# Performance work log

Measured on AMD Instinct MI355X. Metric: run time of the kernel, lower is better.

The kernel has to match this reference:

```python
import jax, jax.numpy as jnp
import numpy as np

B, N, L = 32, 1024, 128
K, D_E, H = 3, 16, 4


def setup_inputs() -> dict:
    key = jax.random.key(0)
    ks = jax.random.split(key, 7)
    return {
        "x": jax.random.normal(ks[0], (B, N, L), jnp.float32),
        # mild scaling on embeddings/projections keeps softmax logits in a sane range
        "psi_emb": jax.random.normal(ks[1], (N, D_E), jnp.float32) * 0.3,
        "psi": jnp.float32(1.0),
        "W_q": jax.random.normal(ks[2], (D_E, H, D_E), jnp.float32) * 0.2,
        "W_k": jax.random.normal(ks[3], (D_E, H, D_E), jnp.float32) * 0.2,
        "attn_alpha": jnp.float32(0.5),
        "F_w": jax.random.normal(ks[4], (H, D_E, K + 1, L), jnp.float32) * 0.1,
        "f_b": jax.random.normal(ks[5], (H, D_E), jnp.float32),
        "head_mix": jnp.ones((H,), jnp.float32),
    }


def reference(x, psi_emb, psi, W_q, W_k, attn_alpha, F_w, f_b, head_mix):
    # x: (B, N, L)
    n = x.shape[1]
    # --- gaussian adjacency: softmax over columns of exp(-psi * ||psi_i - psi_j||^2)
    diff = psi_emb[:, None, :] - psi_emb[None, :, :]          # (N, N, d_e)
    dist2 = jnp.sum(diff * diff, axis=-1)                     # (N, N)
    A_base = jax.nn.softmax(jnp.exp(-psi * dist2), axis=1)    # (N, N)
    # --- per-head attention adjacency
    Q = jnp.einsum('nd,dhm->nhm', psi_emb, W_q)               # (N, H, d_e)
    Kt = jnp.einsum('nd,dhm->nhm', psi_emb, W_k)              # (N, H, d_e)
    scale = 1.0 / jnp.sqrt(jnp.asarray(Q.shape[-1], x.dtype))
    A_attn = jax.nn.softmax(
        jnp.einsum('nhd,mhd->hnm', Q, Kt) * scale, axis=-1)   # (H, N, N)
    # --- sigmoid blend (all heads at once)
    alpha = jax.nn.sigmoid(attn_alpha)
    A_eff = alpha * A_base[None] + (1.0 - alpha) * A_attn     # (H, N, N)
    # --- Chebyshev recursion: T0 = I, T1 = A, Tk = 2 A T_{k-1} - T_{k-2}
    I = jnp.broadcast_to(jnp.eye(n, dtype=x.dtype), A_eff.shape)
    supports = [I, A_eff]
    for _ in range(2, K + 1):
        supports.append(2.0 * jnp.einsum('hnm,hml->hnl', A_eff, supports[-1]) - supports[-2])
    S = jnp.stack(supports, axis=1)                           # (H, K+1, N, N)
    # --- per-node filters
    W_filter = jnp.einsum('nd,hdkl->hnkl', psi_emb, F_w)      # (H, N, K+1, L)
    b_filter = jnp.einsum('nd,hd->hn', psi_emb, f_b)          # (H, N)
    # --- graph conv + node-specific contraction
    x_g = jnp.einsum('hknm,bml->bhknl', S, x)                 # (B, H, K+1, N, L)
    out_h = jnp.einsum('bhknl,hnkl->bhn', x_g, W_filter) + b_filter[None]
    # --- head mixing
    mix_w = jax.nn.softmax(head_mix, axis=0)                  # (H,)
    return jnp.einsum('bhn,h->bn', out_h, mix_w)              # (B, N)
```

## Files before the change

kernel.cpp:

```cpp
#include <hip/hip_runtime.h>
#include <cstdint>

#define NN 1024
#define BB 32
#define LL 128
#define DE 16
#define HH 4
#define K1 4
#define BD 512
#define NS 524288

using bf16x8 = __attribute__((ext_vector_type(8))) short;
using f32x4  = __attribute__((ext_vector_type(4))) float;

__device__ inline unsigned short f2bf(float f) {
    unsigned u = __builtin_bit_cast(unsigned, f);
    u += 0x7FFFu + ((u >> 16) & 1u);
    return (unsigned short)(u >> 16);
}
__device__ inline float bf2f(unsigned short u) {
    return __builtin_bit_cast(float, (unsigned)u << 16);
}

struct LogitsSmem {
    float ejs[64][17];
    float eis[64][17];
    float kjs[64][64];
    float qis[4][64][17];
    float part[4][5][64];
    float wq[1024];
    float wk[1024];
};
struct XtSmem { float xs[64][128]; };

__global__ __launch_bounds__(256) void phase1(
    const float* __restrict__ psi_emb, const float* __restrict__ psi_p,
    const float* __restrict__ W_q, const float* __restrict__ W_k,
    const float* __restrict__ x, const float* __restrict__ F_w,
    short* __restrict__ bnt, short* __restrict__ ant, float* __restrict__ partials,
    short* __restrict__ xt, short* __restrict__ wtt, float* __restrict__ out)
{
    __shared__ __align__(16) char smem_raw[sizeof(LogitsSmem)];
    const int bid = blockIdx.x;
    const int tid = threadIdx.x;

    if (bid < 256) {
        LogitsSmem& S = *(LogitsSmem*)smem_raw;
        const int jb = bid & 15, ib = bid >> 4;
        const int i0 = ib * 64, j0 = jb * 64;
        {
            const int row = tid >> 2, dq = (tid & 3) * 4;
            const float4 vj = *(const float4*)(psi_emb + (j0 + row) * DE + dq);
            S.ejs[row][dq] = vj.x; S.ejs[row][dq + 1] = vj.y;
            S.ejs[row][dq + 2] = vj.z; S.ejs[row][dq + 3] = vj.w;
            const float4 vi = *(const float4*)(psi_emb + (i0 + row) * DE + dq);
            S.eis[row][dq] = vi.x; S.eis[row][dq + 1] = vi.y;
            S.eis[row][dq + 2] = vi.z; S.eis[row][dq + 3] = vi.w;
            *(float4*)&S.wq[tid * 4] = *(const float4*)(W_q + tid * 4);
            *(float4*)&S.wk[tid * 4] = *(const float4*)(W_k + tid * 4);
        }
        __syncthreads();
#pragma unroll
        for (int rep = 0; rep < 16; rep++) {
            const int idx = rep * 256 + tid;
            const int row = idx >> 6, hm = idx & 63;
            float qv = 0.f, kv = 0.f;
#pragma unroll
            for (int d = 0; d < DE; d++) {
                qv += S.eis[row][d] * S.wq[d * 64 + hm];
                kv += S.ejs[row][d] * S.wk[d * 64 + hm];
            }
            S.qis[hm >> 4][row][hm & 15] = qv;
            S.kjs[row][hm] = kv;
        }
        __syncthreads();

        const int i = tid & 63, jg = tid >> 6;
        const float psi = psi_p[0];
        float er[DE];
#pragma unroll
        for (int d = 0; d < DE; d++) er[d] = S.eis[i][d];

        float sb = 0.f, sa[HH] = {0.f, 0.f, 0.f, 0.f};
#pragma unroll
        for (int g = 0; g < 2; g++) {
            unsigned short bw[8];
#pragma unroll
            for (int r = 0; r < 8; r++) {
                const int j = jg * 16 + g * 8 + r;
                float d2 = 0.f;
#pragma unroll
                for (int d = 0; d < DE; d++) { const float t = er[d] - S.ejs[j][d]; d2 += t * t; }
                const float bn = __expf(__expf(-psi * d2));
                sb += bn;
                bw[r] = f2bf(bn);
            }
            uint4 pk;
            pk.x = bw[0] | ((unsigned)bw[1] << 16);
            pk.y = bw[2] | ((unsigned)bw[3] << 16);
            pk.z = bw[4] | ((unsigned)bw[5] << 16);
            pk.w = bw[6] | ((unsigned)bw[7] << 16);
            const size_t toff = (size_t)((j0 + jg * 16 + g * 8) >> 3) * 8192 + (size_t)(i0 + i) * 8;
            *(uint4*)(bnt + toff) = pk;
        }
#pragma unroll
        for (int h = 0; h < HH; h++) {
            float qr[DE];
#pragma unroll
            for (int m = 0; m < DE; m++) qr[m] = S.qis[h][i][m];
#pragma unroll
            for (int g = 0; g < 2; g++) {
                unsigned short aw[8];
#pragma unroll
                for (int r = 0; r < 8; r++) {
                    const int j = jg * 16 + g * 8 + r;
                    float dot = 0.f;
#pragma unroll
                    for (int m = 0; m < DE; m++) dot += qr[m] * S.kjs[j][h * DE + m];
                    const float an = __expf(dot * 0.25f);
                    sa[h] += an;
                    aw[r] = f2bf(an);
                }
                uint4 pk;
                pk.x = aw[0] | ((unsigned)aw[1] << 16);
                pk.y = aw[2] | ((unsigned)aw[3] << 16);
                pk.z = aw[4] | ((unsigned)aw[5] << 16);
                pk.w = aw[6] | ((unsigned)aw[7] << 16);
                const size_t toff = (size_t)((j0 + jg * 16 + g * 8) >> 3) * 8192 + (size_t)(i0 + i) * 8;
                *(uint4*)(ant + (size_t)h * 1048576 + toff) = pk;
            }
        }
        S.part[jg][0][i] = sb;
#pragma unroll
        for (int h = 0; h < HH; h++) S.part[jg][1 + h][i] = sa[h];
        __syncthreads();
        if (tid < 64) {
#pragma unroll
            for (int s = 0; s < 5; s++) {
                const float v = S.part[0][s][tid] + S.part[1][s][tid] +
                                S.part[2][s][tid] + S.part[3][s][tid];
                partials[(size_t)jb * 5120 + (size_t)s * 1024 + i0 + tid] = v;
            }
        }
    } else if (bid < 768) {
        XtSmem& X = *(XtSmem*)smem_raw;
        const int idx = bid - 256;
        const int m0 = (idx & 15) * 64;
        const int b  = idx >> 4;
        for (int i = tid; i < 2048; i += 256) {
            const int row = i >> 5, lq = i & 31;
            *(float4*)&X.xs[row][lq * 4] =
                *(const float4*)(x + ((size_t)(b * NN + m0 + row)) * LL + lq * 4);
        }
        __syncthreads();
        for (int j = tid; j < 1024; j += 256) {
            const int m = j & 63, lc = j >> 6;
            const float* s = &X.xs[m][lc * 8];
            uint4 pk;
            pk.x = f2bf(s[0]) | ((unsigned)f2bf(s[1]) << 16);
            pk.y = f2bf(s[2]) | ((unsigned)f2bf(s[3]) << 16);
            pk.z = f2bf(s[4]) | ((unsigned)f2bf(s[5]) << 16);
            pk.w = f2bf(s[6]) | ((unsigned)f2bf(s[7]) << 16);
            *(uint4*)(xt + (size_t)b * 131072 + (size_t)lc * 8192 + (size_t)(m0 + m) * 8) = pk;
        }
    } else if (bid < 784) {
        const int j = (bid - 768) * 256 + tid;
        const int lc = j >> 8, c = j & 255;
        const int h = c >> 6, k = (c >> 4) & 3, d = c & 15;
        const float* s = F_w + (size_t)((h * DE + d) * K1 + k) * LL + lc * 8;
        uint4 pk;
        pk.x = f2bf(s[0]) | ((unsigned)f2bf(s[1]) << 16);
        pk.y = f2bf(s[2]) | ((unsigned)f2bf(s[3]) << 16);
        pk.z = f2bf(s[4]) | ((unsigned)f2bf(s[5]) << 16);
        pk.w = f2bf(s[6]) | ((unsigned)f2bf(s[7]) << 16);
        *(uint4*)(wtt + (size_t)lc * 2048 + (size_t)c * 8) = pk;
    } else {
        const int idx = (bid - 784) * 256 + tid;
        const float4 z = {0.f, 0.f, 0.f, 0.f};
        *(float4*)(out + (size_t)idx * 8) = z;
        *(float4*)(out + (size_t)idx * 8 + 4) = z;
    }
}

__global__ __launch_bounds__(256) void phase2(
    const short* __restrict__ xt, const short* __restrict__ wtt,
    short* __restrict__ Gt,
    const short* __restrict__ bnt, const short* __restrict__ ant,
    const float* __restrict__ partials, const float* __restrict__ alpha_p,
    short* __restrict__ At)
{
    const int bid = blockIdx.x;
    const int tid = threadIdx.x;
    __shared__ float sums_l[5][64];

    if (bid < 1024) {
        const int cb = bid & 3;
        const int m0 = ((bid >> 2) & 15) * 64;
        const int bp = bid >> 6;
        const int wave = tid >> 6, lane = tid & 63;
        const int b  = bp * 2 + (wave >> 1);
        const int wc = wave & 1;
        const int q = lane >> 4, m16 = lane & 15;
        const short* xb = xt + (size_t)b * 131072;

        f32x4 acc[4][2];
#pragma unroll
        for (int mi = 0; mi < 4; mi++)
#pragma unroll
            for (int ni = 0; ni < 2; ni++) acc[mi][ni] = (f32x4){0.f, 0.f, 0.f, 0.f};

#pragma unroll
        for (int ks = 0; ks < 4; ks++) {
            const int kc = ks * 4 + q;
            bf16x8 a[4], bb[2];
#pragma unroll
            for (int mi = 0; mi < 4; mi++)
                a[mi] = *(const bf16x8*)(xb + (size_t)kc * 8192 + (size_t)(m0 + mi * 16 + m16) * 8);
#pragma unroll
            for (int ni = 0; ni < 2; ni++)
                bb[ni] = *(const bf16x8*)(wtt + (size_t)kc * 2048 +
                                          (size_t)(cb * 64 + wc * 32 + ni * 16 + m16) * 8);
#pragma unroll
            for (int mi = 0; mi < 4; mi++)
#pragma unroll
                for (int ni = 0; ni < 2; ni++)
                    acc[mi][ni] = __builtin_amdgcn_mfma_f32_16x16x32_bf16(a[mi], bb[ni], acc[mi][ni], 0, 0, 0);
        }

#pragma unroll
        for (int ni = 0; ni < 2; ni++) {
            const int cc = cb * 64 + wc * 32 + ni * 16 + m16;
            const int kk = (cc >> 4) & 3, hh = cc >> 6;
            const int col512 = b * 16 + (cc & 15);
            short* gdst = Gt + (size_t)(kk * 4 + hh) * 524288;
#pragma unroll
            for (int mi = 0; mi < 4; mi++) {
                const int row0 = m0 + mi * 16 + q * 4;
                ushort4 pk;
                pk.x = f2bf(acc[mi][ni][0]); pk.y = f2bf(acc[mi][ni][1]);
                pk.z = f2bf(acc[mi][ni][2]); pk.w = f2bf(acc[mi][ni][3]);
                *(ushort4*)(gdst + ((size_t)(row0 >> 3) * 512 + col512) * 8 + (row0 & 7)) = pk;
            }
        }
    } else {
        const int idx = bid - 1024;
        const int jb = idx & 15, ib = idx >> 4;
        const int i0 = ib * 64, j0 = jb * 64;
        const int lane = tid & 63, w = tid >> 6;
        {
            float acc = 0.f;
#pragma unroll
            for (int jb2 = 0; jb2 < 16; jb2++)
                acc += partials[(size_t)jb2 * 5120 + (size_t)w * 1024 + i0 + lane];
            sums_l[w][lane] = acc;
            if (w == 0) {
                float a4 = 0.f;
#pragma unroll
                for (int jb2 = 0; jb2 < 16; jb2++)
                    a4 += partials[(size_t)jb2 * 5120 + 4 * 1024 + i0 + lane];
                sums_l[4][lane] = a4;
            }
        }
        __syncthreads();
        const int i = lane, jg = w;
        const float alpha = 1.f / (1.f + __expf(-alpha_p[0]));
        const float ibs = alpha / sums_l[0][i];
        float ias[HH];
#pragma unroll
        for (int h = 0; h < HH; h++) ias[h] = (1.f - alpha) / sums_l[1 + h][i];

#pragma unroll
        for (int g = 0; g < 2; g++) {
            const size_t toff = (size_t)((j0 + jg * 16 + g * 8) >> 3) * 8192 + (size_t)(i0 + i) * 8;
            const uint4 bp = *(const uint4*)(bnt + toff);
            float bnv[8];
            bnv[0] = bf2f(bp.x & 0xFFFF); bnv[1] = bf2f(bp.x >> 16);
            bnv[2] = bf2f(bp.y & 0xFFFF); bnv[3] = bf2f(bp.y >> 16);
            bnv[4] = bf2f(bp.z & 0xFFFF); bnv[5] = bf2f(bp.z >> 16);
            bnv[6] = bf2f(bp.w & 0xFFFF); bnv[7] = bf2f(bp.w >> 16);
#pragma unroll
            for (int h = 0; h < HH; h++) {
                const uint4 ap = *(const uint4*)(ant + (size_t)h * 1048576 + toff);
                float av[8];
                av[0] = bf2f(ap.x & 0xFFFF); av[1] = bf2f(ap.x >> 16);
                av[2] = bf2f(ap.y & 0xFFFF); av[3] = bf2f(ap.y >> 16);
                av[4] = bf2f(ap.z & 0xFFFF); av[5] = bf2f(ap.z >> 16);
                av[6] = bf2f(ap.w & 0xFFFF); av[7] = bf2f(ap.w >> 16);
                unsigned short ow[8];
#pragma unroll
                for (int r = 0; r < 8; r++) ow[r] = f2bf(ibs * bnv[r] + ias[h] * av[r]);
                uint4 pk;
                pk.x = ow[0] | ((unsigned)ow[1] << 16);
                pk.y = ow[2] | ((unsigned)ow[3] << 16);
                pk.z = ow[4] | ((unsigned)ow[5] << 16);
                pk.w = ow[6] | ((unsigned)ow[7] << 16);
                *(uint4*)(At + (size_t)h * 1048576 + toff) = pk;
            }
        }
    }
}

__global__ __launch_bounds__(256) void gemm_mf(
    const short* __restrict__ At, const short* __restrict__ Bt,
    const short* __restrict__ Pt, const short* __restrict__ Qt,
    short* __restrict__ Ot, float scale, float pc, float qc)
{
    const int bid = blockIdx.x;
    const int h = (bid & 7) >> 1;
    const int tile = ((bid >> 3) << 1) | (bid & 1);
    const int c0 = (tile & 7) * 64;
    const int r0 = (tile >> 3) * 64;

    const short* Ah = At + (size_t)h * 1048576;
    const short* Bh = Bt + (size_t)h * 524288;
    const short* Ph = Pt + (size_t)h * 524288;
    const short* Qh = Qt + (size_t)h * 524288;
    short* Oh = Ot + (size_t)h * 524288;

    const int tid = threadIdx.x;
    const int wave = tid >> 6, lane = tid & 63;
    const int q = lane >> 4, m16 = lane & 15;
    const int wr = wave >> 1, wc = wave & 1;

    const short* Ap = Ah + (size_t)q * 8192 + (size_t)(r0 + wr * 32 + m16) * 8;
    const short* Bp = Bh + (size_t)q * 4096 + (size_t)(c0 + wc * 32 + m16) * 8;

    f32x4 acc[2][2];
#pragma unroll
    for (int mi = 0; mi < 2; mi++)
#pragma unroll
        for (int ni = 0; ni < 2; ni++) acc[mi][ni] = (f32x4){0.f, 0.f, 0.f, 0.f};

#pragma unroll 8
    for (int it = 0; it < 32; it++) {
        const bf16x8 af0 = *(const bf16x8*)(Ap + (size_t)it * 32768);
        const bf16x8 af1 = *(const bf16x8*)(Ap + (size_t)it * 32768 + 128);
        const bf16x8 bf0 = *(const bf16x8*)(Bp + (size_t)it * 16384);
        const bf16x8 bf1 = *(const bf16x8*)(Bp + (size_t)it * 16384 + 128);
        acc[0][0] = __builtin_amdgcn_mfma_f32_16x16x32_bf16(af0, bf0, acc[0][0], 0, 0, 0);
        acc[0][1] = __builtin_amdgcn_mfma_f32_16x16x32_bf16(af0, bf1, acc[0][1], 0, 0, 0);
        acc[1][0] = __builtin_amdgcn_mfma_f32_16x16x32_bf16(af1, bf0, acc[1][0], 0, 0, 0);
        acc[1][1] = __builtin_amdgcn_mfma_f32_16x16x32_bf16(af1, bf1, acc[1][1], 0, 0, 0);
    }

#pragma unroll
    for (int mi = 0; mi < 2; mi++) {
        const int row0 = r0 + wr * 32 + mi * 16 + q * 4;
#pragma unroll
        for (int ni = 0; ni < 2; ni++) {
            const int cc = c0 + wc * 32 + ni * 16 + m16;
            const size_t off = ((size_t)(row0 >> 3) * 512 + cc) * 8 + (row0 & 7);
            const ushort4 pv = *(const ushort4*)(Ph + off);
            float v[4];
            v[0] = scale * acc[mi][ni][0] + pc * bf2f(pv.x);
            v[1] = scale * acc[mi][ni][1] + pc * bf2f(pv.y);
            v[2] = scale * acc[mi][ni][2] + pc * bf2f(pv.z);
            v[3] = scale * acc[mi][ni][3] + pc * bf2f(pv.w);
            if (qc != 0.f) {
                const ushort4 qv = *(const ushort4*)(Qh + off);
                v[0] += qc * bf2f(qv.x); v[1] += qc * bf2f(qv.y);
                v[2] += qc * bf2f(qv.z); v[3] += qc * bf2f(qv.w);
            }
            ushort4 pk;
            pk.x = f2bf(v[0]); pk.y = f2bf(v[1]); pk.z = f2bf(v[2]); pk.w = f2bf(v[3]);
            *(ushort4*)(Oh + off) = pk;
        }
    }
}

__global__ __launch_bounds__(256) void gemm3_out(
    const short* __restrict__ At, const short* __restrict__ Bt,
    const short* __restrict__ Pt, const short* __restrict__ Qt,
    const float* __restrict__ psi_emb, const float* __restrict__ f_b,
    const float* __restrict__ head_mix, float* __restrict__ out)
{
    const int bid = blockIdx.x;
    const int h = (bid & 7) >> 1;
    const int tile = ((bid >> 3) << 1) | (bid & 1);
    const int c0 = (tile & 7) * 64;
    const int r0 = (tile >> 3) * 64;

    const short* Ah = At + (size_t)h * 1048576;
    const short* Bh = Bt + (size_t)h * 524288;
    const short* Ph = Pt + (size_t)h * 524288;
    const short* Qh = Qt + (size_t)h * 524288;

    const int tid = threadIdx.x;
    const int wave = tid >> 6, lane = tid & 63;
    const int q = lane >> 4, m16 = lane & 15;
    const int wr = wave >> 1, wc = wave & 1;

    __shared__ float es[64][17];
    {
        const int row = tid >> 2, dq = (tid & 3) * 4;
        const float4 ev = *(const float4*)(psi_emb + (size_t)(r0 + row) * DE + dq);
        es[row][dq] = ev.x; es[row][dq + 1] = ev.y;
        es[row][dq + 2] = ev.z; es[row][dq + 3] = ev.w;
    }
    __syncthreads();

    const short* Ap = Ah + (size_t)q * 8192 + (size_t)(r0 + wr * 32 + m16) * 8;
    const short* Bp = Bh + (size_t)q * 4096 + (size_t)(c0 + wc * 32 + m16) * 8;

    f32x4 acc[2][2];
#pragma unroll
    for (int mi = 0; mi < 2; mi++)
#pragma unroll
        for (int ni = 0; ni < 2; ni++) acc[mi][ni] = (f32x4){0.f, 0.f, 0.f, 0.f};

#pragma unroll 8
    for (int it = 0; it < 32; it++) {
        const bf16x8 af0 = *(const bf16x8*)(Ap + (size_t)it * 32768);
        const bf16x8 af1 = *(const bf16x8*)(Ap + (size_t)it * 32768 + 128);
        const bf16x8 bf0 = *(const bf16x8*)(Bp + (size_t)it * 16384);
        const bf16x8 bf1 = *(const bf16x8*)(Bp + (size_t)it * 16384 + 128);
        acc[0][0] = __builtin_amdgcn_mfma_f32_16x16x32_bf16(af0, bf0, acc[0][0], 0, 0, 0);
        acc[0][1] = __builtin_amdgcn_mfma_f32_16x16x32_bf16(af0, bf1, acc[0][1], 0, 0, 0);
        acc[1][0] = __builtin_amdgcn_mfma_f32_16x16x32_bf16(af1, bf0, acc[1][0], 0, 0, 0);
        acc[1][1] = __builtin_amdgcn_mfma_f32_16x16x32_bf16(af1, bf1, acc[1][1], 0, 0, 0);
    }

    const float hm0 = head_mix[0], hm1 = head_mix[1], hm2 = head_mix[2], hm3 = head_mix[3];
    const float mx = fmaxf(fmaxf(hm0, hm1), fmaxf(hm2, hm3));
    const float w0 = expf(hm0 - mx), w1 = expf(hm1 - mx), w2 = expf(hm2 - mx), w3 = expf(hm3 - mx);
    const float isum = 1.f / (w0 + w1 + w2 + w3);
    const float mwh = (h == 0 ? w0 : h == 1 ? w1 : h == 2 ? w2 : w3) * isum;
    const float fb = f_b[h * DE + m16];

#pragma unroll
    for (int mi = 0; mi < 2; mi++) {
        const int rloc0 = wr * 32 + mi * 16 + q * 4;
        const int row0 = r0 + rloc0;
#pragma unroll
        for (int ni = 0; ni < 2; ni++) {
            const int cc = c0 + wc * 32 + ni * 16 + m16;
            const int b = cc >> 4;
            const size_t off = ((size_t)(row0 >> 3) * 512 + cc) * 8 + (row0 & 7);
            const ushort4 pv = *(const ushort4*)(Ph + off);
            const ushort4 qv = *(const ushort4*)(Qh + off);
            float v[4];
            v[0] = acc[mi][ni][0] + bf2f(pv.x) - bf2f(qv.x);
            v[1] = acc[mi][ni][1] + bf2f(pv.y) - bf2f(qv.y);
            v[2] = acc[mi][ni][2] + bf2f(pv.z) - bf2f(qv.z);
            v[3] = acc[mi][ni][3] + bf2f(pv.w) - bf2f(qv.w);
#pragma unroll
            for (int r = 0; r < 4; r++) {
                float w = es[rloc0 + r][m16] * (v[r] + fb);
                w += __shfl_xor(w, 1, 64);
                w += __shfl_xor(w, 2, 64);
                w += __shfl_xor(w, 4, 64);
                w += __shfl_xor(w, 8, 64);
                if (m16 == 0)
                    atomicAdd(out + (size_t)b * NN + (row0 + r), mwh * w);
            }
        }
    }
}

extern "C" void kernel_launch(void* const* d_in, const int* in_sizes, int n_in,
                              void* d_out, int out_size, void* d_ws, size_t ws_size,
                              hipStream_t stream)
{
    const float* x          = (const float*)d_in[0];
    const float* psi_emb    = (const float*)d_in[1];
    const float* psi        = (const float*)d_in[2];
    const float* W_q        = (const float*)d_in[3];
    const float* W_k        = (const float*)d_in[4];
    const float* attn_alpha = (const float*)d_in[5];
    const float* F_w        = (const float*)d_in[6];
    const float* f_b        = (const float*)d_in[7];
    const float* head_mix   = (const float*)d_in[8];
    float* out = (float*)d_out;

    short* At  = (short*)d_ws;
    short* xt  = At + 4194304;
    short* wtt = xt + 4194304;
    short* Gt  = wtt + 32768;
    short* b2t = Gt + 8388608;
    short* b1t = b2t + 2097152;
    short* bnt = b1t + 2097152;
    short* ant = bnt + 1048576;
    float* partials = (float*)(ant + 4194304);

    const size_t need_bytes =
        (size_t)(4194304 + 4194304 + 32768 + 8388608 + 2097152 + 2097152 + 1048576 + 4194304) * 2 +
        (size_t)81920 * 4;
    if (ws_size < need_bytes) return;

    phase1<<<800, 256, 0, stream>>>(psi_emb, psi, W_q, W_k, x, F_w,
                                    bnt, ant, partials, xt, wtt, out);
    phase2<<<1280, 256, 0, stream>>>(xt, wtt, Gt, bnt, ant, partials,
                                     attn_alpha, At);

    gemm_mf<<<512, 256, 0, stream>>>(At, Gt + 12 * (size_t)524288, Gt + 8 * (size_t)524288,
                                     Gt , b2t, 2.f, 1.f, 0.f);
    gemm_mf<<<512, 256, 0, stream>>>(At, b2t, Gt + 4 * (size_t)524288,
                                     Gt + 12 * (size_t)524288, b1t, 2.f, 1.f, -1.f);
    gemm3_out<<<512, 256, 0, stream>>>(At, b1t, Gt, b2t, psi_emb, f_b, head_mix, out);
}
```

Before: 149.1 us.

## Stage GEMM operands through LDS with async global_load_lds multi-buffering

Replaces the direct per-lane global loads of the A and B fragments in the two MFMA GEMM kernels with a 4-deep LDS ring buffer filled by global_load_lds (16 bytes per lane), prefetching three k-steps ahead and using explicit vmcnt waits plus barriers. This shares each tile load across the block's waves instead of every wave loading its own fragments from global memory, and hides load latency behind the MFMAs. Epilogue reads of the P/Q operands switch to nontemporal loads. It adds two barriers per k-step and hand-tuned waitcnt values that rely on the exact count of outstanding loads.

After: 150.5 us. No clear change (+1.0%).

```diff
diff --git a/kernel.cpp b/kernel.cpp
--- a/kernel.cpp
+++ b/kernel.cpp
@@ -12,6 +12,7 @@
 
 using bf16x8 = __attribute__((ext_vector_type(8))) short;
 using f32x4  = __attribute__((ext_vector_type(4))) float;
+using u16x4  = __attribute__((ext_vector_type(4))) unsigned short;
 
 __device__ inline unsigned short f2bf(float f) {
     unsigned u = __builtin_bit_cast(unsigned, f);
@@ -21,6 +22,11 @@
 __device__ inline float bf2f(unsigned short u) {
     return __builtin_bit_cast(float, (unsigned)u << 16);
 }
+
+typedef const __attribute__((address_space(1))) void gas_void;
+typedef __attribute__((address_space(3))) void las_void;
+#define GLD16(gsrc, ldst) \
+    __builtin_amdgcn_global_load_lds((gas_void*)(gsrc), (las_void*)(ldst), 16, 0, 0)
 
 struct LogitsSmem {
     float ejs[64][17];
@@ -322,8 +328,18 @@
     const int q = lane >> 4, m16 = lane & 15;
     const int wr = wave >> 1, wc = wave & 1;
 
-    const short* Ap = Ah + (size_t)q * 8192 + (size_t)(r0 + wr * 32 + m16) * 8;
-    const short* Bp = Bh + (size_t)q * 4096 + (size_t)(c0 + wc * 32 + m16) * 8;
+    __shared__ __align__(16) short Asm[4][4][64][8];
+    __shared__ __align__(16) short Bsm[4][4][64][8];
+
+    const char* Abase = (const char*)Ah + (size_t)r0 * 16;
+    const char* Bbase = (const char*)Bh + (size_t)c0 * 16;
+
+#define STAGE_MF(itc, bufc)                                                     \
+    do {                                                                        \
+        const size_t ko_ = (size_t)((itc) * 4 + wave);                          \
+        GLD16(Abase + ko_ * 16384 + (size_t)lane * 16, &Asm[bufc][wave][0][0]); \
+        GLD16(Bbase + ko_ * 8192  + (size_t)lane * 16, &Bsm[bufc][wave][0][0]); \
+    } while (0)
 
     f32x4 acc[2][2];
 #pragma unroll
@@ -331,17 +347,32 @@
 #pragma unroll
         for (int ni = 0; ni < 2; ni++) acc[mi][ni] = (f32x4){0.f, 0.f, 0.f, 0.f};
 
-#pragma unroll 8
-    for (int it = 0; it < 32; it++) {
-        const bf16x8 af0 = *(const bf16x8*)(Ap + (size_t)it * 32768);
-        const bf16x8 af1 = *(const bf16x8*)(Ap + (size_t)it * 32768 + 128);
-        const bf16x8 bf0 = *(const bf16x8*)(Bp + (size_t)it * 16384);
-        const bf16x8 bf1 = *(const bf16x8*)(Bp + (size_t)it * 16384 + 128);
+    STAGE_MF(0, 0);
+    STAGE_MF(1, 1);
+    STAGE_MF(2, 2);
+
+#pragma unroll
+    for (int it = 0; it < 32; ++it) {
+        if (it < 29) STAGE_MF(it + 3, (it + 3) & 3);
+        if (it < 29)      asm volatile("s_waitcnt vmcnt(6)" ::: "memory");
+        else if (it == 29) asm volatile("s_waitcnt vmcnt(4)" ::: "memory");
+        else if (it == 30) asm volatile("s_waitcnt vmcnt(2)" ::: "memory");
+        else               asm volatile("s_waitcnt vmcnt(0)" ::: "memory");
+        __builtin_amdgcn_s_barrier();
+
+        const int b = it & 3;
+        const bf16x8 af0 = *(const bf16x8*)&Asm[b][q][wr * 32 + m16][0];
+        const bf16x8 af1 = *(const bf16x8*)&Asm[b][q][wr * 32 + 16 + m16][0];
+        const bf16x8 bf0 = *(const bf16x8*)&Bsm[b][q][wc * 32 + m16][0];
+        const bf16x8 bf1 = *(const bf16x8*)&Bsm[b][q][wc * 32 + 16 + m16][0];
         acc[0][0] = __builtin_amdgcn_mfma_f32_16x16x32_bf16(af0, bf0, acc[0][0], 0, 0, 0);
         acc[0][1] = __builtin_amdgcn_mfma_f32_16x16x32_bf16(af0, bf1, acc[0][1], 0, 0, 0);
         acc[1][0] = __builtin_amdgcn_mfma_f32_16x16x32_bf16(af1, bf0, acc[1][0], 0, 0, 0);
         acc[1][1] = __builtin_amdgcn_mfma_f32_16x16x32_bf16(af1, bf1, acc[1][1], 0, 0, 0);
-    }
+
+        __builtin_amdgcn_s_barrier();
+    }
+#undef STAGE_MF
 
 #pragma unroll
     for (int mi = 0; mi < 2; mi++) {
@@ -350,16 +381,16 @@
         for (int ni = 0; ni < 2; ni++) {
             const int cc = c0 + wc * 32 + ni * 16 + m16;
             const size_t off = ((size_t)(row0 >> 3) * 512 + cc) * 8 + (row0 & 7);
-            const ushort4 pv = *(const ushort4*)(Ph + off);
+            const u16x4 pv = __builtin_nontemporal_load((const u16x4*)(Ph + off));
             float v[4];
-            v[0] = scale * acc[mi][ni][0] + pc * bf2f(pv.x);
-            v[1] = scale * acc[mi][ni][1] + pc * bf2f(pv.y);
-            v[2] = scale * acc[mi][ni][2] + pc * bf2f(pv.z);
-            v[3] = scale * acc[mi][ni][3] + pc * bf2f(pv.w);
+            v[0] = scale * acc[mi][ni][0] + pc * bf2f(pv[0]);
+            v[1] = scale * acc[mi][ni][1] + pc * bf2f(pv[1]);
+            v[2] = scale * acc[mi][ni][2] + pc * bf2f(pv[2]);
+            v[3] = scale * acc[mi][ni][3] + pc * bf2f(pv[3]);
             if (qc != 0.f) {
-                const ushort4 qv = *(const ushort4*)(Qh + off);
-                v[0] += qc * bf2f(qv.x); v[1] += qc * bf2f(qv.y);
-                v[2] += qc * bf2f(qv.z); v[3] += qc * bf2f(qv.w);
+                const u16x4 qv = __builtin_nontemporal_load((const u16x4*)(Qh + off));
+                v[0] += qc * bf2f(qv[0]); v[1] += qc * bf2f(qv[1]);
+                v[2] += qc * bf2f(qv[2]); v[3] += qc * bf2f(qv[3]);
             }
             ushort4 pk;
             pk.x = f2bf(v[0]); pk.y = f2bf(v[1]); pk.z = f2bf(v[2]); pk.w = f2bf(v[3]);
@@ -391,6 +422,9 @@
     const int wr = wave >> 1, wc = wave & 1;
 
     __shared__ float es[64][17];
+    __shared__ __align__(16) short Asm[4][4][64][8];
+    __shared__ __align__(16) short Bsm[4][4][64][8];
+
     {
         const int row = tid >> 2, dq = (tid & 3) * 4;
         const float4 ev = *(const float4*)(psi_emb + (size_t)(r0 + row) * DE + dq);
@@ -399,8 +433,15 @@
     }
     __syncthreads();
 
-    const short* Ap = Ah + (size_t)q * 8192 + (size_t)(r0 + wr * 32 + m16) * 8;
-    const short* Bp = Bh + (size_t)q * 4096 + (size_t)(c0 + wc * 32 + m16) * 8;
+    const char* Abase = (const char*)Ah + (size_t)r0 * 16;
+    const char* Bbase = (const char*)Bh + (size_t)c0 * 16;
+
+#define STAGE_G3(itc, bufc)                                                     \
+    do {                                                                        \
+        const size_t ko_ = (size_t)((itc) * 4 + wave);                          \
+        GLD16(Abase + ko_ * 16384 + (size_t)lane * 16, &Asm[bufc][wave][0][0]); \
+        GLD16(Bbase + ko_ * 8192  + (size_t)lane * 16, &Bsm[bufc][wave][0][0]); \
+    } while (0)
 
     f32x4 acc[2][2];
 #pragma unroll
@@ -408,17 +449,32 @@
 #pragma unroll
         for (int ni = 0; ni < 2; ni++) acc[mi][ni] = (f32x4){0.f, 0.f, 0.f, 0.f};
 
-#pragma unroll 8
-    for (int it = 0; it < 32; it++) {
-        const bf16x8 af0 = *(const bf16x8*)(Ap + (size_t)it * 32768);
-        const bf16x8 af1 = *(const bf16x8*)(Ap + (size_t)it * 32768 + 128);
-        const bf16x8 bf0 = *(const bf16x8*)(Bp + (size_t)it * 16384);
-        const bf16x8 bf1 = *(const bf16x8*)(Bp + (size_t)it * 16384 + 128);
+    STAGE_G3(0, 0);
+    STAGE_G3(1, 1);
+    STAGE_G3(2, 2);
+
+#pragma unroll
+    for (int it = 0; it < 32; ++it) {
+        if (it < 29) STAGE_G3(it + 3, (it + 3) & 3);
+        if (it < 29)      asm volatile("s_waitcnt vmcnt(6)" ::: "memory");
+        else if (it == 29) asm volatile("s_waitcnt vmcnt(4)" ::: "memory");
+        else if (it == 30) asm volatile("s_waitcnt vmcnt(2)" ::: "memory");
+        else               asm volatile("s_waitcnt vmcnt(0)" ::: "memory");
+        __builtin_amdgcn_s_barrier();
+
+        const int b = it & 3;
+        const bf16x8 af0 = *(const bf16x8*)&Asm[b][q][wr * 32 + m16][0];
+        const bf16x8 af1 = *(const bf16x8*)&Asm[b][q][wr * 32 + 16 + m16][0];
+        const bf16x8 bf0 = *(const bf16x8*)&Bsm[b][q][wc * 32 + m16][0];
+        const bf16x8 bf1 = *(const bf16x8*)&Bsm[b][q][wc * 32 + 16 + m16][0];
         acc[0][0] = __builtin_amdgcn_mfma_f32_16x16x32_bf16(af0, bf0, acc[0][0], 0, 0, 0);
         acc[0][1] = __builtin_amdgcn_mfma_f32_16x16x32_bf16(af0, bf1, acc[0][1], 0, 0, 0);
         acc[1][0] = __builtin_amdgcn_mfma_f32_16x16x32_bf16(af1, bf0, acc[1][0], 0, 0, 0);
         acc[1][1] = __builtin_amdgcn_mfma_f32_16x16x32_bf16(af1, bf1, acc[1][1], 0, 0, 0);
-    }
+
+        __builtin_amdgcn_s_barrier();
+    }
+#undef STAGE_G3
 
     const float hm0 = head_mix[0], hm1 = head_mix[1], hm2 = head_mix[2], hm3 = head_mix[3];
     const float mx = fmaxf(fmaxf(hm0, hm1), fmaxf(hm2, hm3));
@@ -436,13 +492,13 @@
             const int cc = c0 + wc * 32 + ni * 16 + m16;
             const int b = cc >> 4;
             const size_t off = ((size_t)(row0 >> 3) * 512 + cc) * 8 + (row0 & 7);
-            const ushort4 pv = *(const ushort4*)(Ph + off);
-            const ushort4 qv = *(const ushort4*)(Qh + off);
+            const u16x4 pv = __builtin_nontemporal_load((const u16x4*)(Ph + off));
+            const u16x4 qv = __builtin_nontemporal_load((const u16x4*)(Qh + off));
             float v[4];
-            v[0] = acc[mi][ni][0] + bf2f(pv.x) - bf2f(qv.x);
-            v[1] = acc[mi][ni][1] + bf2f(pv.y) - bf2f(qv.y);
-            v[2] = acc[mi][ni][2] + bf2f(pv.z) - bf2f(qv.z);
-            v[3] = acc[mi][ni][3] + bf2f(pv.w) - bf2f(qv.w);
+            v[0] = acc[mi][ni][0] + bf2f(pv[0]) - bf2f(qv[0]);
+            v[1] = acc[mi][ni][1] + bf2f(pv[1]) - bf2f(qv[1]);
+            v[2] = acc[mi][ni][2] + bf2f(pv[2]) - bf2f(qv[2]);
+            v[3] = acc[mi][ni][3] + bf2f(pv[3]) - bf2f(qv[3]);
 #pragma unroll
             for (int r = 0; r < 4; r++) {
                 float w = es[rloc0 + r][m16] * (v[r] + fb);
```
